# Performance work log

Measured on AMD Instinct MI355X. Metric: run time of the kernel, lower is better.

## Reference

```python
import jax, jax.numpy as jnp
import numpy as np

B, T, D = 64, 64, 64
E, HA, HB, OUT = 128, 128, 128, 1
SHORT = 2


def _rn(k, shape, scale=0.05):
    return jax.random.normal(k, shape, dtype=jnp.float32) * scale


def setup_inputs() -> dict:
    key = jax.random.key(0)
    ks = jax.random.split(key, 18)
    return {
        "x": jax.random.normal(ks[0], (B, T, D), dtype=jnp.float32),
        "W_emb": _rn(ks[1], (E, D)), "b_emb": _rn(ks[2], (E,)),
        "Wi_a": _rn(ks[3], (3 * HA, E)), "Wh_a": _rn(ks[4], (3 * HA, HA)),
        "bi_a": _rn(ks[5], (3 * HA,)), "bh_a": _rn(ks[6], (3 * HA,)),
        "Wi_b": _rn(ks[7], (3 * HB, E)), "Wh_b": _rn(ks[8], (3 * HB, HB)),
        "bi_b": _rn(ks[9], (3 * HB,)), "bh_b": _rn(ks[10], (3 * HB,)),
        "Wa": _rn(ks[11], (1, HA)), "ba": _rn(ks[12], (1,)),
        "Wb": _rn(ks[13], (E, HB)), "bb": _rn(ks[14], (E,)),
        "Wo": _rn(ks[15], (OUT, E)), "bo": _rn(ks[16], (OUT,)),
        "short": SHORT,
    }


def _gru_cell(x, h, Wi, Wh, bi, bh):
    # PyTorch GRU cell: gates ordered (r, z, n)
    gi = x @ Wi.T + bi
    gh = h @ Wh.T + bh
    ir, iz, in_ = jnp.split(gi, 3, axis=-1)
    hr, hz, hn = jnp.split(gh, 3, axis=-1)
    r = jax.nn.sigmoid(ir + hr)
    z = jax.nn.sigmoid(iz + hz)
    n = jnp.tanh(in_ + r * hn)
    return (1.0 - z) * n + z * h


def _forward(x, W_emb, b_emb, Wi_a, Wh_a, bi_a, bh_a, Wi_b, Wh_b, bi_b, bh_b,
             Wa, ba, Wb, bb, Wo, bo, short):
    Bn, Tn = x.shape[0], x.shape[1]
    temp = jnp.transpose(x, (1, 0, 2))            # [T, B, D]
    emb = temp @ W_emb.T + b_emb                  # [T, B, E]
    P = Tn - 1                                    # prefix p handles att_timesteps t = p+1
    S = Tn - 1                                    # max reversed-prefix length
    p_idx = jnp.arange(P)
    h0a = jnp.zeros((P, Bn, Wh_a.shape[1]), x.dtype)
    h0b = jnp.zeros((P, Bn, Wh_b.shape[1]), x.dtype)

    # All prefixes at once: for prefix p, reversed input at step s is emb[p - s].
    def step(carry, s):
        ha, hb = carry
        j = jnp.clip(p_idx - s, 0, Tn - 1)        # [P]
        e_in = emb[j]                             # [P, B, E]
        x_in = temp[j]                            # [P, B, D]
        na = _gru_cell(e_in, ha, Wi_a, Wh_a, bi_a, bh_a)
        nb = _gru_cell(e_in, hb, Wi_b, Wh_b, bi_b, bh_b)
        valid = (p_idx >= s)[:, None, None]
        ha = jnp.where(valid, na, ha)
        hb = jnp.where(valid, nb, hb)
        return (ha, hb), (ha, hb, e_in, x_in)

    _, (Ha, Hb, Eg, Xg) = jax.lax.scan(step, (h0a, h0b), jnp.arange(S))
    Ha = 0.5 * Ha                                 # reverse_h_a * 0.5, [S, P, B, HA]
    Hb = 0.5 * Hb                                 # reverse_h_b * 0.5, [S, P, B, HB]

    mask = p_idx[None, :] >= jnp.arange(S)[:, None]   # [S, P] valid scan steps
    preA = jnp.einsum('spbh,h->spb', Ha, Wa[0]) + ba[0]
    preA = jnp.where(mask[:, :, None], preA, -jnp.inf)
    alpha = jax.nn.softmax(preA, axis=0)              # softmax over prefix positions
    beta = jnp.tanh(jnp.einsum('spbh,eh->spbe', Hb, Wb) + bb)  # [S, P, B, E]

    # context: c[p] = sum_s alpha * beta * emb[p-s]  (softmax is order-invariant)
    c = jnp.einsum('spb,spbe->pbe', alpha, beta * Eg)          # [P, B, E]
    pred = c @ Wo.T + bo                                        # [P, B, 1]

    # interpretability weights: e = (beta * w_out) @ W_emb, f = alpha*e*x, g = mean over prefix
    e_chain = jnp.einsum('spbe,ed->spbd', beta * Wo[0], W_emb)  # [S, P, B, D]
    f = alpha[..., None] * e_chain * Xg
    g = jnp.sum(f, axis=0) / (p_idx[:, None, None] + 1.0)       # mean over t = p+1 steps

    pred = jnp.transpose(pred[short + 1:], (1, 0, 2))           # [B, T-2-short, 1]
    weight = jnp.transpose(g[short + 1:], (1, 0, 2))            # [B, T-2-short, D]
    return pred, weight


def reference(x, W_emb, b_emb, Wi_a, Wh_a, bi_a, bh_a, Wi_b, Wh_b, bi_b, bh_b,
              Wa, ba, Wb, bb, Wo, bo, short):
    return _forward(x, W_emb, b_emb, Wi_a, Wh_a, bi_a, bh_a, Wi_b, Wh_b, bi_b,
                    bh_b, Wa, ba, Wb, bb, Wo, bo, short)
```

## Files before the change

### kernel.cpp

```cpp
#include <hip/hip_runtime.h>
#include <hip/hip_bf16.h>
#include <math.h>

#define B_ 64
#define T_ 64
#define D_ 64
#define PMIN 3
#define NPOUT 60
#define NCHUNK 4

#define LOG2E     1.4426950408889634f
#define TWOLOG2E  2.8853900817779268f

typedef __hip_bfloat16 bf16;
typedef __attribute__((ext_vector_type(4))) short s16x4;
typedef __attribute__((ext_vector_type(8))) short s16x8;
typedef __attribute__((ext_vector_type(4))) float f32x4;

#define OFF_EMB   0
#define OFF_WIC2  524288
#define OFF_XT    622592
#define OFF_GIPK  884736
#define OFF_WPK   2457600
#define OFF_BPPK  2506752
#define OFF_WMPK  2514944
#define OFF_WALPK 2519040
#define OFF_FLAG  2520064

__device__ __forceinline__ float bf2f(unsigned short u) {
    union { float f; unsigned u32; } x; x.u32 = ((unsigned)u) << 16; return x.f;
}
__device__ __forceinline__ unsigned short f2bf(float f) {
    union { float f; unsigned u; } x; x.f = f;
    unsigned r = x.u + 0x7FFFu + ((x.u >> 16) & 1u);
    return (unsigned short)(r >> 16);
}
__device__ __forceinline__ float LDF(const void* p, int i, int flag) {
    return flag ? ((const float*)p)[i] : bf2f(((const unsigned short*)p)[i]);
}
__device__ __forceinline__ float sig2(float xneg) {
    return __builtin_amdgcn_rcpf(1.f + __builtin_exp2f(xneg));
}
__device__ __forceinline__ float tanh2(float x2) {
    return 1.f - 2.f * __builtin_amdgcn_rcpf(1.f + __builtin_exp2f(x2));
}
__device__ __forceinline__ int kpi(int s) {
    return (s & ~31) | ((s & 1) << 4) | ((s & 31) >> 1);
}

__global__ void detect_dtype(const unsigned short* xr, int* flag)
{
    int tid = threadIdx.x;
    int bad = 0;
    for (int i = tid; i < 4096; i += 256) {
        int ex = (xr[i] >> 7) & 0xFF;
        if (ex >= 140) bad++;
    }
    __shared__ int s[256];
    s[tid] = bad;
    __syncthreads();
    for (int st = 128; st > 0; st >>= 1) {
        if (tid < st) s[tid] += s[tid + st];
        __syncthreads();
    }
    if (tid == 0) *flag = (s[0] > 4) ? 1 : 0;
}

__global__ void prep_all(const void* p_x, const void* p_wemb,
                         const void* p_wia, const void* p_wib,
                         const void* p_wha, const void* p_whb,
                         const void* p_wa, const void* p_wb, const void* p_wo,
                         float* ws, const int* flagp)
{
    const int flag = *flagp;
    int id = blockIdx.x * 256 + threadIdx.x;
    if (id < 98304) {
        float v = (id < 49152) ? LDF(p_wia, id, flag)
                               : LDF(p_wib, id - 49152, flag);
        ws[OFF_WIC2 + id] = v;
    } else if (id < 360448) {
        int id5 = id - 98304;
        int b = id5 & 63, d = (id5 >> 6) & 63, t = id5 >> 12;
        ws[OFF_XT + id5] = LDF(p_x, (b * 64 + t) * 64 + d, flag);
    } else if (id < 458752) {
        unsigned short* wpk = (unsigned short*)(ws + OFF_WPK);
        int id3 = id - 360448;
        int w = id3 / 12288, r1 = id3 % 12288;
        int nt = r1 / 2048, r2 = r1 % 2048;
        int kt = r2 / 512, r3 = r2 % 512;
        int lane = r3 >> 3, j = r3 & 7;
        int cell = w >> 2, wv = w & 3;
        int gate = nt >> 1, tt = nt & 1;
        int g = gate * 128 + wv * 32 + tt * 16 + (lane & 15);
        int k = kpi(kt * 32 + (lane >> 4) * 8 + j);
        float sc = (gate < 2) ? -LOG2E : TWOLOG2E;
        wpk[id3] = f2bf(sc * LDF(cell ? p_whb : p_wha, g * 128 + k, flag));
    } else if (id < 475136) {
        unsigned short* bpk = (unsigned short*)(ws + OFF_BPPK);
        int id4 = id - 458752;
        int w = id4 / 2048, r = id4 % 2048;
        int kt = r / 512, lane = (r % 512) >> 3, j = r & 7;
        int e = w * 16 + (lane & 15);
        int k = kpi(kt * 32 + (lane >> 4) * 8 + j);
        bpk[id4] = f2bf(LOG2E * LDF(p_wb, e * 128 + k, flag));
    } else if (id < 483328) {
        unsigned short* wmk = (unsigned short*)(ws + OFF_WMPK);
        int id6 = id - 475136;
        int nt = id6 / 2048, r = id6 % 2048;
        int kt = r / 512, lane = (r % 512) >> 3, j = r & 7;
        int d = nt * 16 + (lane & 15);
        int e = kt * 32 + (lane >> 4) * 8 + j;
        wmk[id6] = f2bf(LDF(p_wo, e, flag) * LDF(p_wemb, e * 64 + d, flag));
    } else {
        unsigned short* alk = (unsigned short*)(ws + OFF_WALPK);
        int id7 = id - 483328;
        int kt = id7 / 512, lane = (id7 % 512) >> 3, j = id7 & 7;
        int k = kpi(kt * 32 + (lane >> 4) * 8 + j);
        alk[id7] = ((lane & 15) == 0) ? f2bf(0.5f * LOG2E * LDF(p_wa, k, flag))
                                      : (unsigned short)0;
    }
}

__global__ void prep_gi(float* ws, const void* p_x, const void* p_wemb,
                        const void* p_bemb, const void* p_bia, const void* p_bha,
                        const void* p_bib, const void* p_bhb, const int* flagp)
{
    const int flag = *flagp;
    unsigned short* gipk = (unsigned short*)(ws + OFF_GIPK);
    int t = blockIdx.x >> 3;
    int chunk = blockIdx.x & 7;
    int b0 = chunk * 8;
    int tid = threadIdx.x;
    __shared__ __align__(16) float sX[8][64];
    __shared__ __align__(16) float sWe[128][64];
    __shared__ __align__(16) float semT2[8][132];
    __shared__ __align__(16) unsigned short stg[6144];

    for (int i = tid; i < 512; i += 256) {
        int r = i >> 6, d = i & 63;
        sX[r][d] = LDF(p_x, ((b0 + r) * 64 + t) * 64 + d, flag);
    }
    for (int i = tid; i < 8192; i += 256)
        sWe[i >> 6][i & 63] = LDF(p_wemb, i, flag);
    __syncthreads();

    #pragma unroll
    for (int q = 0; q < 4; q++) {
        int o = tid + q * 256;
        int e = o & 127, r = o >> 7;
        float acc = LDF(p_bemb, e, flag);
        #pragma unroll
        for (int d = 0; d < 64; d += 4) {
            f32x4 xv = *(const f32x4*)&sX[r][d];
            f32x4 wv = *(const f32x4*)&sWe[e][d];
            acc += xv[0]*wv[0] + xv[1]*wv[1] + xv[2]*wv[2] + xv[3]*wv[3];
        }
        semT2[r][e] = acc;
        ws[OFF_EMB + (size_t)((t * 64 + b0 + r) * 128) + e] = acc;
    }
    __syncthreads();

    float acc3[3][8];
    #pragma unroll
    for (int g3 = 0; g3 < 3; g3++)
        #pragma unroll
        for (int r = 0; r < 8; r++) acc3[g3][r] = 0.f;
    const float* w2 = ws + OFF_WIC2;
    #pragma unroll 2
    for (int e0 = 0; e0 < 128; e0 += 4) {
        f32x4 wv0 = *(const f32x4*)(w2 + (size_t)(tid      ) * 128 + e0);
        f32x4 wv1 = *(const f32x4*)(w2 + (size_t)(tid + 256) * 128 + e0);
        f32x4 wv2 = *(const f32x4*)(w2 + (size_t)(tid + 512) * 128 + e0);
        f32x4 h[8];
        #pragma unroll
        for (int r = 0; r < 8; r++) h[r] = *(const f32x4*)&semT2[r][e0];
        #pragma unroll
        for (int r = 0; r < 8; r++)
            #pragma unroll
            for (int c = 0; c < 4; c++) {
                acc3[0][r] += wv0[c] * h[r][c];
                acc3[1][r] += wv1[c] * h[r][c];
                acc3[2][r] += wv2[c] * h[r][c];
            }
    }
    #pragma unroll
    for (int g3 = 0; g3 < 3; g3++) {
        int g = tid + g3 * 256;
        int cellg = g / 384, gr = g % 384;
        int gate = gr / 128, kh = gr % 128;
        int wvp = kh / 32, tt2 = (kh % 32) / 16, l15p = kh % 16;
        int wq = cellg * 4 + wvp;
        float bias = LDF(cellg ? p_bib : p_bia, gr, flag);
        if (gate < 2) bias += LDF(cellg ? p_bhb : p_bha, gr, flag);
        float sc = (gate < 2) ? -LOG2E : TWOLOG2E;
        #pragma unroll
        for (int r = 0; r < 8; r++) {
            float v = sc * (acc3[g3][r] + bias);
            int lane2 = (r >> 2) * 16 + l15p;
            int slot = gate * 8 + tt2 * 4 + (r & 3);
            stg[(wq * 32 + lane2) * 24 + slot] = f2bf(v);
        }
    }
    __syncthreads();
    const uint4* s4 = (const uint4*)stg;
    const int c16 = chunk >> 1, rhalf = chunk & 1;
    uint4* d4 = (uint4*)(gipk + (size_t)(t * 4 + c16) * 12288);
    for (int i = tid; i < 768; i += 256) {
        int wq = i / 96, rem = i % 96;
        d4[wq * 192 + rhalf * 96 + rem] = s4[i];
    }
}


__launch_bounds__(512, 2)
__global__ void chain_kernel(const float* ws, void* outv, const int* flagp,
                             const void* p_bha, const void* p_bhb,
                             const void* p_bb, const void* p_ba,
                             const void* p_bo, const void* p_wo)
{
    const int p = PMIN + (NPOUT - 1) - (int)blockIdx.x / NCHUNK;
    const int chunk = (int)blockIdx.x % NCHUNK;
    const int tid = threadIdx.x;
    const int lane = tid & 63;
    const int w = tid >> 6;
    const int cell = w >> 2;
    const int wv = w & 3;
    const int l15 = lane & 15;
    const int quad = lane >> 4;

    __shared__ __align__(16) short hbf[2][2][16][136];
    __shared__ __align__(16) short betbf[2][16][136];
    __shared__ __align__(16) short sWm[4][4][64][8];
    __shared__ float weLds[2][16];

    const unsigned short* gipk = (const unsigned short*)(ws + OFF_GIPK);
    const unsigned short* wpk  = (const unsigned short*)(ws + OFF_WPK);
    const unsigned short* bpk  = (const unsigned short*)(ws + OFF_BPPK);
    const unsigned short* alk  = (const unsigned short*)(ws + OFF_WALPK);
    const int flag = *flagp;

    {
        const int* s2 = (const int*)(ws + OFF_WMPK);
        int* d2 = (int*)&sWm[0][0][0][0];
        for (int i = tid; i < 4096; i += 512) d2[i] = s2[i];
        int* hz = (int*)&hbf[0][0][0][0];
        for (int i = tid; i < 4352; i += 512) hz[i] = 0;
        int* bz = (int*)&betbf[0][0][0];
        for (int i = tid; i < 2176; i += 512) bz[i] = 0;
    }

    s16x8 wB[6][4];
    #pragma unroll
    for (int nt = 0; nt < 6; nt++)
        #pragma unroll
        for (int kt = 0; kt < 4; kt++)
            wB[nt][kt] = *(const s16x8*)(wpk + (((w * 6 + nt) * 4 + kt) * 64 + lane) * 8);
    s16x8 bBp[4], wAl[4];
    #pragma unroll
    for (int kt = 0; kt < 4; kt++) {
        bBp[kt] = *(const s16x8*)(bpk + ((w * 4 + kt) * 64 + lane) * 8);
        wAl[kt] = *(const s16x8*)(alk + (kt * 64 + lane) * 8);
    }

    const float bhnS0 = TWOLOG2E *
        LDF(cell ? p_bhb : p_bha, 256 + wv * 32 + l15, flag);
    const float bhnS1 = TWOLOG2E *
        LDF(cell ? p_bhb : p_bha, 256 + wv * 32 + 16 + l15, flag);
    const float bbE2 = TWOLOG2E * LDF(p_bb, w * 16 + l15, flag);
    const float bafS = LOG2E * LDF(p_ba, 0, flag);
    const float bof  = LDF(p_bo, 0, flag);

    float h_old[8];
    #pragma unroll
    for (int i = 0; i < 8; i++) h_old[i] = 0.f;
    float accR[9];
    #pragma unroll
    for (int i = 0; i < 9; i++) accR[i] = 0.f;

    f32x4 xvP = (f32x4){0.f,0.f,0.f,0.f};
    f32x4 em0P = (f32x4){0.f,0.f,0.f,0.f};
    f32x4 em1P = (f32x4){0.f,0.f,0.f,0.f};

    auto phaseC = [&](int dbufP) {
        if (w < 4) {
            f32x4 ec = (f32x4){0.f,0.f,0.f,0.f};
            #pragma unroll
            for (int kt = 0; kt < 4; kt++) {
                s16x8 a = *(const s16x8*)&betbf[dbufP][l15][kt * 32 + quad * 8];
                s16x8 bw = *(const s16x8*)&sWm[w][kt][lane][0];
                ec = __builtin_amdgcn_mfma_f32_16x16x32_bf16(a, bw, ec, 0, 0, 0);
            }
            #pragma unroll
            for (int reg = 0; reg < 4; reg++) {
                float we = weLds[dbufP][quad * 4 + reg];
                accR[4 + reg] += we;
                accR[reg] += we * ec[reg] * xvP[reg];
            }
        } else {
            const int row = quad * 4 + (w - 4);
            float we = weLds[dbufP][row];
            accR[8] += we;
            const short* bp2 = &betbf[dbufP][row][l15 * 8];
            s16x4 blo = *(const s16x4*)bp2;
            s16x4 bhi = *(const s16x4*)(bp2 + 4);
            #pragma unroll
            for (int v = 0; v < 4; v++)
                accR[v] += we * bf2f((unsigned short)blo[v]) * em0P[v];
            #pragma unroll
            for (int v = 0; v < 4; v++)
                accR[4 + v] += we * bf2f((unsigned short)bhi[v]) * em1P[v];
        }
    };

    __syncthreads();

    for (int it = 0; it <= p + 1; it++) {
        const int j = p - it;
        const int jp = j + 1;
        const bool doGru = (j >= 0);
        const int cur = it & 1;
        const int nxt = cur ^ 1;
        const int dbuf = it & 1;

        s16x8 giv[3];
        if (doGru) {
            const unsigned short* gp0 =
                gipk + ((((size_t)j * 4 + chunk) * 8 + w) * 64 + lane) * 24;
            giv[0] = *(const s16x8*)(gp0);
            giv[1] = *(const s16x8*)(gp0 + 8);
            giv[2] = *(const s16x8*)(gp0 + 16);
        }

        if (it > 1) phaseC(dbuf ^ 1);

        if (it > 0) {
            if (w < 4) {
                xvP = *(const f32x4*)(ws + OFF_XT + ((size_t)jp * 64 + w * 16 + l15) * 64
                                      + chunk * 16 + quad * 4);
            } else {
                const int row = quad * 4 + (w - 4);
                const float* ep = ws + OFF_EMB
                                  + ((size_t)jp * 64 + chunk * 16 + row) * 128 + l15 * 8;
                em0P = *(const f32x4*)ep;
                em1P = *(const f32x4*)(ep + 4);
            }
        }

        f32x4 Cg[6], Cbp, Cal;
        #pragma unroll
        for (int nt = 0; nt < 6; nt++) Cg[nt] = (f32x4){0.f,0.f,0.f,0.f};
        Cbp = (f32x4){0.f,0.f,0.f,0.f};
        Cal = (f32x4){0.f,0.f,0.f,0.f};

        #pragma unroll
        for (int kt = 0; kt < 4; kt++) {
            s16x8 aB = *(const s16x8*)&hbf[cur][1][l15][kt * 32 + quad * 8];
            s16x8 aA;
            if (cell == 0 || w == 7) aA = *(const s16x8*)&hbf[cur][0][l15][kt * 32 + quad * 8];
            else aA = aB;
            s16x8 aOwn = cell ? aB : aA;
            #pragma unroll
            for (int nt = 0; nt < 6; nt++)
                Cg[nt] = __builtin_amdgcn_mfma_f32_16x16x32_bf16(aOwn, wB[nt][kt], Cg[nt], 0, 0, 0);
            Cbp = __builtin_amdgcn_mfma_f32_16x16x32_bf16(aB, bBp[kt], Cbp, 0, 0, 0);
            if (w == 7)
                Cal = __builtin_amdgcn_mfma_f32_16x16x32_bf16(aA, wAl[kt], Cal, 0, 0, 0);
        }

        if (w == 7 && l15 == 0) {
            #pragma unroll
            for (int reg = 0; reg < 4; reg++)
                weLds[dbuf][quad * 4 + reg] =
                    __builtin_exp2f(fminf(Cal[reg] + bafS, 86.f));
        }
        if (doGru) {
            #pragma unroll
            for (int reg = 0; reg < 4; reg++) {
                float rr0 = sig2(bf2f((unsigned short)giv[0][reg]) + Cg[0][reg]);
                float zz0 = sig2(bf2f((unsigned short)giv[1][reg]) + Cg[2][reg]);
                float nn0 = tanh2(bf2f((unsigned short)giv[2][reg])
                                  + rr0 * (Cg[4][reg] + bhnS0));
                float h0 = (1.f - zz0) * nn0 + zz0 * h_old[reg];
                h_old[reg] = h0;
                float rr1 = sig2(bf2f((unsigned short)giv[0][4 + reg]) + Cg[1][reg]);
                float zz1 = sig2(bf2f((unsigned short)giv[1][4 + reg]) + Cg[3][reg]);
                float nn1 = tanh2(bf2f((unsigned short)giv[2][4 + reg])
                                  + rr1 * (Cg[5][reg] + bhnS1));
                float h1 = (1.f - zz1) * nn1 + zz1 * h_old[4 + reg];
                h_old[4 + reg] = h1;
                unsigned pk;
                asm("v_cvt_pk_bf16_f32 %0, %1, %2" : "=v"(pk) : "v"(h0), "v"(h1));
                *(unsigned*)&hbf[nxt][cell][quad * 4 + reg][wv * 32 + l15 * 2] = pk;
            }
        }
        {
            #pragma unroll
            for (int reg = 0; reg < 4; reg++) {
                float bv = tanh2(Cbp[reg] + bbE2);
                betbf[dbuf][quad * 4 + reg][w * 16 + l15] = (short)f2bf(bv);
            }
        }

        __syncthreads();
    }

    phaseC((p + 1) & 1);

    if (w >= 4) {
        const int row = quad * 4 + (w - 4);
        float wo8[8];
        if (flag) {
            const float* wp = (const float*)p_wo + l15 * 8;
            #pragma unroll
            for (int v = 0; v < 8; v++) wo8[v] = wp[v];
        } else {
            const unsigned short* wp = (const unsigned short*)p_wo + l15 * 8;
            #pragma unroll
            for (int v = 0; v < 8; v++) wo8[v] = bf2f(wp[v]);
        }
        float part = 0.f;
        #pragma unroll
        for (int v = 0; v < 8; v++) part += accR[v] * wo8[v];
        part += __shfl_xor(part, 1);
        part += __shfl_xor(part, 2);
        part += __shfl_xor(part, 4);
        part += __shfl_xor(part, 8);
        if (l15 == 0) {
            int bglob = chunk * 16 + row;
            float pr = part / accR[8] + bof;
            size_t oi = (size_t)bglob * NPOUT + (p - PMIN);
            if (flag) ((float*)outv)[oi] = pr;
            else      ((bf16*)outv)[oi] = __float2bfloat16(pr);
        }
    } else {
        const float invt = 1.f / (float)(p + 1);
        #pragma unroll
        for (int reg = 0; reg < 4; reg++) {
            int row = quad * 4 + reg;
            int bglob = chunk * 16 + row;
            float gv = accR[reg] / accR[4 + reg] * invt;
            size_t oi = (size_t)B_ * NPOUT
                      + ((size_t)bglob * NPOUT + (p - PMIN)) * 64 + w * 16 + l15;
            if (flag) ((float*)outv)[oi] = gv;
            else      ((bf16*)outv)[oi] = __float2bfloat16(gv);
        }
    }
}

extern "C" void kernel_launch(void* const* d_in, const int* in_sizes, int n_in,
                              void* d_out, int out_size, void* d_ws, size_t ws_size,
                              hipStream_t stream)
{
    float* ws = (float*)d_ws;
    int* flagp = (int*)(ws + OFF_FLAG);

    hipLaunchKernelGGL(detect_dtype, dim3(1), dim3(256), 0, stream,
                       (const unsigned short*)d_in[0], flagp);
    hipLaunchKernelGGL(prep_all, dim3(1896), dim3(256), 0, stream,
                       d_in[0], d_in[1], d_in[3], d_in[7], d_in[4], d_in[8],
                       d_in[11], d_in[13], d_in[15], ws, flagp);
    hipLaunchKernelGGL(prep_gi, dim3(512), dim3(256), 0, stream,
                       ws, d_in[0], d_in[1], d_in[2], d_in[5], d_in[6],
                       d_in[9], d_in[10], flagp);
    hipLaunchKernelGGL(chain_kernel, dim3(NPOUT * NCHUNK), dim3(512), 0, stream,
                       ws, d_out, flagp,
                       d_in[6], d_in[10], d_in[14], d_in[12], d_in[16], d_in[15]);
}
```

Baseline: 315.9 us.

## Prefetch next-step GRU input gates and relax per-step barrier in recurrence loop

Loads the precomputed input-gate values for step j-1 at the end of each iteration and before the loop, instead of at the top of the iteration where the load latency sits on the critical path. Replaces __syncthreads with an LDS-only waitcnt plus s_barrier, so outstanding global prefetches can stay in flight across the barrier. Also skips the MFMA and beta/alpha work at it==0, where the hidden state is zero and the results are never consumed, and skips the GRU MFMAs on the final non-GRU step. This adds register pressure from the held prefetch and relies on correct manual wait counts.

New measurement: 311.1 us. No clear change (-1.5%).

```diff
diff --git a/kernel.cpp b/kernel.cpp
--- a/kernel.cpp
+++ b/kernel.cpp
@@ -277,6 +277,14 @@
     #pragma unroll
     for (int i = 0; i < 9; i++) accR[i] = 0.f;
 
+    s16x8 givP[3];
+    {
+        const unsigned short* gp0 =
+            gipk + ((((size_t)p * 4 + chunk) * 8 + w) * 64 + lane) * 24;
+        givP[0] = *(const s16x8*)(gp0);
+        givP[1] = *(const s16x8*)(gp0 + 8);
+        givP[2] = *(const s16x8*)(gp0 + 16);
+    }
     f32x4 xvP = (f32x4){0.f,0.f,0.f,0.f};
     f32x4 em0P = (f32x4){0.f,0.f,0.f,0.f};
     f32x4 em1P = (f32x4){0.f,0.f,0.f,0.f};
@@ -316,24 +324,15 @@
 
     for (int it = 0; it <= p + 1; it++) {
         const int j = p - it;
-        const int jp = j + 1;
         const bool doGru = (j >= 0);
         const int cur = it & 1;
         const int nxt = cur ^ 1;
         const int dbuf = it & 1;
 
-        s16x8 giv[3];
-        if (doGru) {
-            const unsigned short* gp0 =
-                gipk + ((((size_t)j * 4 + chunk) * 8 + w) * 64 + lane) * 24;
-            giv[0] = *(const s16x8*)(gp0);
-            giv[1] = *(const s16x8*)(gp0 + 8);
-            giv[2] = *(const s16x8*)(gp0 + 16);
-        }
-
         if (it > 1) phaseC(dbuf ^ 1);
 
-        if (it > 0) {
+        if (it >= 1) {
+            const int jp = j + 1;
             if (w < 4) {
                 xvP = *(const f32x4*)(ws + OFF_XT + ((size_t)jp * 64 + w * 16 + l15) * 64
                                       + chunk * 16 + quad * 4);
@@ -352,39 +351,52 @@
         Cbp = (f32x4){0.f,0.f,0.f,0.f};
         Cal = (f32x4){0.f,0.f,0.f,0.f};
 
-        #pragma unroll
-        for (int kt = 0; kt < 4; kt++) {
-            s16x8 aB = *(const s16x8*)&hbf[cur][1][l15][kt * 32 + quad * 8];
-            s16x8 aA;
-            if (cell == 0 || w == 7) aA = *(const s16x8*)&hbf[cur][0][l15][kt * 32 + quad * 8];
-            else aA = aB;
-            s16x8 aOwn = cell ? aB : aA;
-            #pragma unroll
-            for (int nt = 0; nt < 6; nt++)
-                Cg[nt] = __builtin_amdgcn_mfma_f32_16x16x32_bf16(aOwn, wB[nt][kt], Cg[nt], 0, 0, 0);
-            Cbp = __builtin_amdgcn_mfma_f32_16x16x32_bf16(aB, bBp[kt], Cbp, 0, 0, 0);
-            if (w == 7)
-                Cal = __builtin_amdgcn_mfma_f32_16x16x32_bf16(aA, wAl[kt], Cal, 0, 0, 0);
-        }
-
-        if (w == 7 && l15 == 0) {
-            #pragma unroll
-            for (int reg = 0; reg < 4; reg++)
-                weLds[dbuf][quad * 4 + reg] =
-                    __builtin_exp2f(fminf(Cal[reg] + bafS, 86.f));
+        if (it > 0) {
+            #pragma unroll
+            for (int kt = 0; kt < 4; kt++) {
+                s16x8 aB = *(const s16x8*)&hbf[cur][1][l15][kt * 32 + quad * 8];
+                s16x8 aA;
+                if (cell == 0 || w == 7) aA = *(const s16x8*)&hbf[cur][0][l15][kt * 32 + quad * 8];
+                else aA = aB;
+                if (doGru) {
+                    s16x8 aOwn = cell ? aB : aA;
+                    #pragma unroll
+                    for (int nt = 0; nt < 6; nt++)
+                        Cg[nt] = __builtin_amdgcn_mfma_f32_16x16x32_bf16(aOwn, wB[nt][kt], Cg[nt], 0, 0, 0);
+                }
+                Cbp = __builtin_amdgcn_mfma_f32_16x16x32_bf16(aB, bBp[kt], Cbp, 0, 0, 0);
+                if (w == 7)
+                    Cal = __builtin_amdgcn_mfma_f32_16x16x32_bf16(aA, wAl[kt], Cal, 0, 0, 0);
+            }
+        }
+
+        if (it > 0) {
+            if (w == 7 && l15 == 0) {
+                #pragma unroll
+                for (int reg = 0; reg < 4; reg++)
+                    weLds[dbuf][quad * 4 + reg] =
+                        __builtin_exp2f(fminf(Cal[reg] + bafS, 86.f));
+            }
+            {
+                #pragma unroll
+                for (int reg = 0; reg < 4; reg++) {
+                    float bv = tanh2(Cbp[reg] + bbE2);
+                    betbf[dbuf][quad * 4 + reg][w * 16 + l15] = (short)f2bf(bv);
+                }
+            }
         }
         if (doGru) {
             #pragma unroll
             for (int reg = 0; reg < 4; reg++) {
-                float rr0 = sig2(bf2f((unsigned short)giv[0][reg]) + Cg[0][reg]);
-                float zz0 = sig2(bf2f((unsigned short)giv[1][reg]) + Cg[2][reg]);
-                float nn0 = tanh2(bf2f((unsigned short)giv[2][reg])
+                float rr0 = sig2(bf2f((unsigned short)givP[0][reg]) + Cg[0][reg]);
+                float zz0 = sig2(bf2f((unsigned short)givP[1][reg]) + Cg[2][reg]);
+                float nn0 = tanh2(bf2f((unsigned short)givP[2][reg])
                                   + rr0 * (Cg[4][reg] + bhnS0));
                 float h0 = (1.f - zz0) * nn0 + zz0 * h_old[reg];
                 h_old[reg] = h0;
-                float rr1 = sig2(bf2f((unsigned short)giv[0][4 + reg]) + Cg[1][reg]);
-                float zz1 = sig2(bf2f((unsigned short)giv[1][4 + reg]) + Cg[3][reg]);
-                float nn1 = tanh2(bf2f((unsigned short)giv[2][4 + reg])
+                float rr1 = sig2(bf2f((unsigned short)givP[0][4 + reg]) + Cg[1][reg]);
+                float zz1 = sig2(bf2f((unsigned short)givP[1][4 + reg]) + Cg[3][reg]);
+                float nn1 = tanh2(bf2f((unsigned short)givP[2][4 + reg])
                                   + rr1 * (Cg[5][reg] + bhnS1));
                 float h1 = (1.f - zz1) * nn1 + zz1 * h_old[4 + reg];
                 h_old[4 + reg] = h1;
@@ -393,15 +405,18 @@
                 *(unsigned*)&hbf[nxt][cell][quad * 4 + reg][wv * 32 + l15 * 2] = pk;
             }
         }
-        {
-            #pragma unroll
-            for (int reg = 0; reg < 4; reg++) {
-                float bv = tanh2(Cbp[reg] + bbE2);
-                betbf[dbuf][quad * 4 + reg][w * 16 + l15] = (short)f2bf(bv);
-            }
-        }
-
-        __syncthreads();
+
+        if (it <= p - 1) {
+            const unsigned short* gp0 =
+                gipk + ((((size_t)(j - 1) * 4 + chunk) * 8 + w) * 64 + lane) * 24;
+            givP[0] = *(const s16x8*)(gp0);
+            givP[1] = *(const s16x8*)(gp0 + 8);
+            givP[2] = *(const s16x8*)(gp0 + 16);
+        }
+
+        asm volatile("s_waitcnt lgkmcnt(0)" ::: "memory");
+        __builtin_amdgcn_s_barrier();
+        __builtin_amdgcn_sched_barrier(0);
     }
 
     phaseC((p + 1) & 1);
```

## Tile input-gate weight matmul through shared memory in prep_gi

Applied to the files above, without the earlier changes.

Replaces the per-thread strided global reads of the 768x128 input-gate weight matrix with twelve 64-row tiles staged into LDS. The LDS is shared with the embedding-weight buffer, and the 8-row by 3-gate per-thread work split becomes 2 rows per thread per tile. The aim is coalesced global loads in place of row-strided uncoalesced ones. In exchange it adds many more barriers and tile reloads per block.

New measurement: 321.4 us. Within noise of the previous version (+1.8%).

```diff
diff --git a/kernel.cpp b/kernel.cpp
--- a/kernel.cpp
+++ b/kernel.cpp
@@ -131,71 +131,83 @@
     int chunk = blockIdx.x & 7;
     int b0 = chunk * 8;
     int tid = threadIdx.x;
-    __shared__ __align__(16) float sX[8][64];
-    __shared__ __align__(16) float sWe[128][64];
+
+    __shared__ __align__(16) float regionA[9216];
     __shared__ __align__(16) float semT2[8][132];
     __shared__ __align__(16) unsigned short stg[6144];
 
-    for (int i = tid; i < 512; i += 256) {
-        int r = i >> 6, d = i & 63;
-        sX[r][d] = LDF(p_x, ((b0 + r) * 64 + t) * 64 + d, flag);
-    }
-    for (int i = tid; i < 8192; i += 256)
-        sWe[i >> 6][i & 63] = LDF(p_wemb, i, flag);
-    __syncthreads();
-
-    #pragma unroll
-    for (int q = 0; q < 4; q++) {
-        int o = tid + q * 256;
-        int e = o & 127, r = o >> 7;
-        float acc = LDF(p_bemb, e, flag);
-        #pragma unroll
-        for (int d = 0; d < 64; d += 4) {
-            f32x4 xv = *(const f32x4*)&sX[r][d];
-            f32x4 wv = *(const f32x4*)&sWe[e][d];
-            acc += xv[0]*wv[0] + xv[1]*wv[1] + xv[2]*wv[2] + xv[3]*wv[3];
-        }
-        semT2[r][e] = acc;
-        ws[OFF_EMB + (size_t)((t * 64 + b0 + r) * 128) + e] = acc;
-    }
-    __syncthreads();
-
-    float acc3[3][8];
-    #pragma unroll
-    for (int g3 = 0; g3 < 3; g3++)
-        #pragma unroll
-        for (int r = 0; r < 8; r++) acc3[g3][r] = 0.f;
+    {
+        float (*sWe)[64] = (float(*)[64])regionA;
+        float (*sX)[64]  = (float(*)[64])(regionA + 8192);
+        for (int i = tid; i < 512; i += 256) {
+            int r = i >> 6, d = i & 63;
+            sX[r][d] = LDF(p_x, ((b0 + r) * 64 + t) * 64 + d, flag);
+        }
+        for (int i = tid; i < 8192; i += 256)
+            sWe[i >> 6][i & 63] = LDF(p_wemb, i, flag);
+        __syncthreads();
+
+        #pragma unroll
+        for (int q = 0; q < 4; q++) {
+            int o = tid + q * 256;
+            int e = o & 127, r = o >> 7;
+            float acc = LDF(p_bemb, e, flag);
+            #pragma unroll
+            for (int d = 0; d < 64; d += 4) {
+                f32x4 xv = *(const f32x4*)&sX[r][d];
+                f32x4 wv = *(const f32x4*)&sWe[e][d];
+                acc += xv[0]*wv[0] + xv[1]*wv[1] + xv[2]*wv[2] + xv[3]*wv[3];
+            }
+            semT2[r][e] = acc;
+            ws[OFF_EMB + (size_t)((t * 64 + b0 + r) * 128) + e] = acc;
+        }
+    }
+
     const float* w2 = ws + OFF_WIC2;
-    #pragma unroll 2
-    for (int e0 = 0; e0 < 128; e0 += 4) {
-        f32x4 wv0 = *(const f32x4*)(w2 + (size_t)(tid      ) * 128 + e0);
-        f32x4 wv1 = *(const f32x4*)(w2 + (size_t)(tid + 256) * 128 + e0);
-        f32x4 wv2 = *(const f32x4*)(w2 + (size_t)(tid + 512) * 128 + e0);
-        f32x4 h[8];
-        #pragma unroll
-        for (int r = 0; r < 8; r++) h[r] = *(const f32x4*)&semT2[r][e0];
-        #pragma unroll
-        for (int r = 0; r < 8; r++)
-            #pragma unroll
-            for (int c = 0; c < 4; c++) {
-                acc3[0][r] += wv0[c] * h[r][c];
-                acc3[1][r] += wv1[c] * h[r][c];
-                acc3[2][r] += wv2[c] * h[r][c];
-            }
-    }
-    #pragma unroll
-    for (int g3 = 0; g3 < 3; g3++) {
-        int g = tid + g3 * 256;
-        int cellg = g / 384, gr = g % 384;
-        int gate = gr / 128, kh = gr % 128;
-        int wvp = kh / 32, tt2 = (kh % 32) / 16, l15p = kh % 16;
-        int wq = cellg * 4 + wvp;
+    const int gl64 = tid >> 2;
+    const int rq = tid & 3;
+    for (int tile = 0; tile < 12; tile++) {
+        __syncthreads();
+        const int g0 = tile * 64;
+        for (int idx = tid; idx < 8192; idx += 256) {
+            int gl = idx >> 7, e = idx & 127;
+            regionA[gl * 132 + e] = w2[(size_t)(g0 + gl) * 128 + e];
+        }
+        __syncthreads();
+
+        float a0 = 0.f, a1 = 0.f;
+        const float* wrow = regionA + gl64 * 132;
+        const float* h0p = &semT2[rq * 2][0];
+        const float* h1p = &semT2[rq * 2 + 1][0];
+        #pragma unroll 4
+        for (int e0 = 0; e0 < 128; e0 += 4) {
+            f32x4 wv  = *(const f32x4*)(wrow + e0);
+            f32x4 hv0 = *(const f32x4*)(h0p + e0);
+            f32x4 hv1 = *(const f32x4*)(h1p + e0);
+            a0 += wv[0] * hv0[0]; a0 += wv[1] * hv0[1];
+            a0 += wv[2] * hv0[2]; a0 += wv[3] * hv0[3];
+            a1 += wv[0] * hv1[0]; a1 += wv[1] * hv1[1];
+            a1 += wv[2] * hv1[2]; a1 += wv[3] * hv1[3];
+        }
+
+        const int g = g0 + gl64;
+        const int cellg = g / 384, gr = g % 384;
+        const int gate = gr / 128, kh = gr % 128;
+        const int wvp = kh / 32, tt2 = (kh % 32) / 16, l15p = kh % 16;
+        const int wq = cellg * 4 + wvp;
         float bias = LDF(cellg ? p_bib : p_bia, gr, flag);
         if (gate < 2) bias += LDF(cellg ? p_bhb : p_bha, gr, flag);
-        float sc = (gate < 2) ? -LOG2E : TWOLOG2E;
-        #pragma unroll
-        for (int r = 0; r < 8; r++) {
-            float v = sc * (acc3[g3][r] + bias);
+        const float sc = (gate < 2) ? -LOG2E : TWOLOG2E;
+        {
+            int r = rq * 2;
+            float v = sc * (a0 + bias);
+            int lane2 = (r >> 2) * 16 + l15p;
+            int slot = gate * 8 + tt2 * 4 + (r & 3);
+            stg[(wq * 32 + lane2) * 24 + slot] = f2bf(v);
+        }
+        {
+            int r = rq * 2 + 1;
+            float v = sc * (a1 + bias);
             int lane2 = (r >> 2) * 16 + l15p;
             int slot = gate * 8 + tt2 * 4 + (r & 3);
             stg[(wq * 32 + lane2) * 24 + slot] = f2bf(v);
```
